# Kernel optimization log

Hardware: AMD Instinct MI355X
Metric: run time of the kernel (lower is better)

## Reference

```python
import jax, jax.numpy as jnp
import numpy as np

MASK_THR = 0.005   # cfg.mask_thr
SIGMA = 2.0        # cfg.sigma (gaussian kernel)
N, G, H, W = 500, 128, 200, 304


def setup_inputs() -> dict:
    key = jax.random.key(0)
    k1, k2, k3, k4, k5, k6 = jax.random.split(key, 6)
    return {
        "cate_scores": jax.random.uniform(k1, (N,), jnp.float32),
        "seg_preds_x": jax.random.uniform(k2, (G, H, W), jnp.float32),
        "seg_preds_y": jax.random.uniform(k3, (G, H, W), jnp.float32),
        "cate_labels": jax.random.randint(k4, (N,), 0, 80),
        "x_inds": jax.random.randint(k5, (N,), 0, G),
        "y_inds": jax.random.randint(k6, (N,), 0, G),
    }


def reference(cate_scores, seg_preds_x, seg_preds_y, cate_labels, x_inds, y_inds):
    # --- SOLO decoupled mask decoding: irregular grid-index gather ---
    mask_x = seg_preds_x[x_inds]                 # [N,H,W]
    mask_y = seg_preds_y[y_inds]                 # [N,H,W]
    soft = mask_x * mask_y                       # seg_masks_soft
    hard = (soft > MASK_THR).astype(soft.dtype)  # seg_masks (binary)
    sum_masks = hard.sum((1, 2))                 # [N] mask areas
    # mask-quality rescoring
    seg_score = (soft * hard).sum((1, 2)) / jnp.maximum(sum_masks, 1.0)
    scores = cate_scores * seg_score

    # --- Matrix NMS (gaussian kernel) ---
    flat = hard.reshape(N, -1)                   # [N, H*W]
    inter = flat @ flat.T                        # [N,N] intersection areas
    union = sum_masks[:, None] + sum_masks[None, :] - inter
    iou = jnp.triu(inter / jnp.maximum(union, 1e-6), k=1)
    label_eq = jnp.triu((cate_labels[:, None] == cate_labels[None, :]).astype(soft.dtype), k=1)
    decay_iou = iou * label_eq                   # same-class IoU, upper tri
    comp_iou = decay_iou.max(0)                  # [N] max IoU with higher-scored same-class mask
    decay_matrix = jnp.exp(-SIGMA * decay_iou ** 2)
    comp_matrix = jnp.exp(-SIGMA * comp_iou ** 2)[:, None]  # expand(n,n).T in torch
    decay_coef = (decay_matrix / comp_matrix).min(0)         # [N]
    return scores * decay_coef
```

## Files before the change

kernel.cpp:

```cpp
#include <hip/hip_runtime.h>


#define N_DET 500
#define HW    (200 * 304)
#define TILE  64
#define NT    (HW / TILE)
#define NWORDS NT
#define NW2   (NWORDS / 2)
#define LSTR  65
#define MASK_THR 0.005f
#define SIGMA 2.0f

__global__ __launch_bounds__(512) void maskgen_kernel(
    const float* __restrict__ seg_x, const float* __restrict__ seg_y,
    const int* __restrict__ x_inds, const int* __restrict__ y_inds,
    unsigned long long* __restrict__ packed,
    float* __restrict__ part_sum,
    int*   __restrict__ part_cnt)
{
    __shared__ float sx[128 * LSTR];
    __shared__ float sy[128 * LSTR];
    const int t   = blockIdx.x;
    const int tid = threadIdx.x;
    const int base_g = t * TILE;

    for (int e = tid; e < 128 * 16; e += 512) {
        const int r  = e >> 4;
        const int c4 = (e & 15) << 2;
        const float4 vx = *(const float4*)(seg_x + (size_t)r * HW + base_g + c4);
        const float4 vy = *(const float4*)(seg_y + (size_t)r * HW + base_g + c4);
        float* dx = sx + r * LSTR + c4;
        float* dy = sy + r * LSTR + c4;
        dx[0] = vx.x; dx[1] = vx.y; dx[2] = vx.z; dx[3] = vx.w;
        dy[0] = vy.x; dy[1] = vy.y; dy[2] = vy.z; dy[3] = vy.w;
    }
    __syncthreads();

    const int n = tid;
    if (n < N_DET) {
        const float* __restrict__ rx = sx + x_inds[n] * LSTR;
        const float* __restrict__ ry = sy + y_inds[n] * LSTR;
        float ssum = 0.0f;
        int   cnt  = 0;
        unsigned int lo = 0u, hi = 0u;
        #pragma unroll
        for (int p = 0; p < 32; ++p) {
            const float v = rx[p] * ry[p];
            if (v > MASK_THR) { ssum += v; ++cnt; lo |= (1u << p); }
        }
        #pragma unroll
        for (int p = 0; p < 32; ++p) {
            const float v = rx[32 + p] * ry[32 + p];
            if (v > MASK_THR) { ssum += v; ++cnt; hi |= (1u << p); }
        }
        packed[(size_t)n * NWORDS + t] = ((unsigned long long)hi << 32) | lo;
        part_sum[(size_t)t * N_DET + n] = ssum;
        part_cnt[(size_t)t * N_DET + n] = cnt;
    }
}

__global__ __launch_bounds__(64) void finalize_kernel(
    const float* __restrict__ part_sum, const int* __restrict__ part_cnt,
    const float* __restrict__ cate_scores,
    float* __restrict__ sum_masks, float* __restrict__ scores)
{
    const int n    = blockIdx.x;
    const int lane = threadIdx.x;
    float S = 0.0f; int C = 0;
    for (int t = lane; t < NT; t += 64) {
        S += part_sum[(size_t)t * N_DET + n];
        C += part_cnt[(size_t)t * N_DET + n];
    }
    #pragma unroll
    for (int off = 32; off; off >>= 1) {
        S += __shfl_down(S, off);
        C += __shfl_down(C, off);
    }
    if (lane == 0) {
        const float sm = (float)C;
        sum_masks[n] = sm;
        scores[n] = cate_scores[n] * (S / fmaxf(sm, 1.0f));
    }
}

__global__ __launch_bounds__(256) void pair_iou_kernel(
    const unsigned long long* __restrict__ packed,
    const float* __restrict__ sum_masks,
    const int* __restrict__ labels,
    float* __restrict__ d2col,
    float* __restrict__ comp2)
{
    const int j   = blockIdx.x;
    const int tid = threadIdx.x;
    const int lane = tid & 63, wav = tid >> 6;

    __shared__ int   s_lab[N_DET];
    __shared__ float s_sm[N_DET];
    __shared__ int   s_list[N_DET];
    __shared__ int   s_cnt;
    __shared__ float s_max[4];

    if (tid == 0) s_cnt = 0;
    for (int i = tid; i < N_DET; i += 256) {
        s_lab[i] = labels[i];
        s_sm[i]  = sum_masks[i];
        d2col[(size_t)j * N_DET + i] = 0.0f;
    }
    __syncthreads();

    const int   lj = s_lab[j];
    const float sj = s_sm[j];
    for (int i = tid; i < j; i += 256)
        if (s_lab[i] == lj) { const int p = atomicAdd(&s_cnt, 1); s_list[p] = i; }
    __syncthreads();
    const int cnt = s_cnt;

    const ulonglong2* __restrict__ pj2 = (const ulonglong2*)(packed + (size_t)j * NWORDS);
    ulonglong2 bj[8];
    #pragma unroll
    for (int t = 0; t < 8; ++t) {
        const int w = lane + (t << 6);
        if (w < NW2) bj[t] = pj2[w];
        else { bj[t].x = 0ull; bj[t].y = 0ull; }
    }

    float wmax = 0.0f;
    for (int p = wav; p < cnt; p += 4) {
        const int i = s_list[p];
        const ulonglong2* __restrict__ pi2 = (const ulonglong2*)(packed + (size_t)i * NWORDS);
        int part = 0;
        #pragma unroll
        for (int t = 0; t < 8; ++t) {
            const int w = lane + (t << 6);
            if (w < NW2) {
                const ulonglong2 a = pi2[w];
                part += __popcll(a.x & bj[t].x) + __popcll(a.y & bj[t].y);
            }
        }
        #pragma unroll
        for (int off = 32; off; off >>= 1) part += __shfl_down(part, off);
        if (lane == 0) {
            const float uni = s_sm[i] + sj - (float)part;
            const float iou = (float)part / fmaxf(uni, 1e-6f);
            d2col[(size_t)j * N_DET + i] = iou * iou;
            wmax = fmaxf(wmax, iou);
        }
    }
    if (lane == 0) s_max[wav] = wmax;
    __syncthreads();
    if (tid == 0) {
        const float c = fmaxf(fmaxf(s_max[0], s_max[1]), fmaxf(s_max[2], s_max[3]));
        comp2[j] = c * c;
    }
}

__global__ __launch_bounds__(64) void decay_kernel(
    const float* __restrict__ d2col,
    const float* __restrict__ comp2,
    const float* __restrict__ scores,
    float* __restrict__ out)
{
    const int j = blockIdx.x;
    const int lane = threadIdx.x;
    float m = 1e30f;
    for (int i = lane; i < N_DET; i += 64)
        m = fminf(m, comp2[i] - d2col[(size_t)j * N_DET + i]);
    #pragma unroll
    for (int off = 32; off; off >>= 1)
        m = fminf(m, __shfl_down(m, off));
    if (lane == 0) out[j] = scores[j] * expf(SIGMA * m);
}

extern "C" void kernel_launch(void* const* d_in, const int* in_sizes, int n_in,
                              void* d_out, int out_size, void* d_ws, size_t ws_size,
                              hipStream_t stream) {
    const float* cate_scores = (const float*)d_in[0];
    const float* seg_x       = (const float*)d_in[1];
    const float* seg_y       = (const float*)d_in[2];
    const int*   labels      = (const int*)d_in[3];
    const int*   x_inds      = (const int*)d_in[4];
    const int*   y_inds      = (const int*)d_in[5];
    float* out = (float*)d_out;

    char* ws = (char*)d_ws;
    unsigned long long* packed = (unsigned long long*)(ws + 0);
    float* d2col     = (float*)(ws + 3800000);
    float* part_sum  = (float*)(ws + 4800000);
    int*   part_cnt  = (int*)  (ws + 6700000);
    float* scores    = (float*)(ws + 8600000);
    float* comp2     = (float*)(ws + 8602048);
    float* sum_masks = (float*)(ws + 8604096);

    maskgen_kernel <<<NT, 512, 0, stream>>>(seg_x, seg_y, x_inds, y_inds,
                                            packed, part_sum, part_cnt);
    finalize_kernel<<<N_DET, 64, 0, stream>>>(part_sum, part_cnt, cate_scores,
                                              sum_masks, scores);
    pair_iou_kernel<<<N_DET, 256, 0, stream>>>(packed, sum_masks, labels, d2col, comp2);
    decay_kernel   <<<N_DET, 64, 0, stream>>>(d2col, comp2, scores, out);
}
```

Measured before the change: 135.1 us.

## Transpose packed mask bitsets to tile-major layout and derive counts via popcount

Packed mask bitsets move from detection-major to tile-major order with a padded stride of 512, so the mask generation kernel writes one coalesced row per tile instead of scattered per-detection writes. The separate count buffer is dropped: mask areas are now recomputed in the finalize kernel by popcounting the packed words. The finalize kernel is also regrouped so each block reduces 64 detections across 8 waves. The trade-off is that the pair-IoU kernel now reads single 64-bit words at a large stride per lane rather than contiguous 128-bit vectors, which may make its memory access less coalesced.

Result: slower. 173.5 us (+28.5%).

```diff
diff --git a/kernel.cpp b/kernel.cpp
--- a/kernel.cpp
+++ b/kernel.cpp
@@ -5,8 +5,7 @@
 #define HW    (200 * 304)
 #define TILE  64
 #define NT    (HW / TILE)
-#define NWORDS NT
-#define NW2   (NWORDS / 2)
+#define PSTR  512
 #define LSTR  65
 #define MASK_THR 0.005f
 #define SIGMA 2.0f
@@ -14,21 +13,20 @@
 __global__ __launch_bounds__(512) void maskgen_kernel(
     const float* __restrict__ seg_x, const float* __restrict__ seg_y,
     const int* __restrict__ x_inds, const int* __restrict__ y_inds,
-    unsigned long long* __restrict__ packed,
-    float* __restrict__ part_sum,
-    int*   __restrict__ part_cnt)
+    unsigned long long* __restrict__ packed_t,
+    float* __restrict__ part_sum)
 {
     __shared__ float sx[128 * LSTR];
     __shared__ float sy[128 * LSTR];
     const int t   = blockIdx.x;
     const int tid = threadIdx.x;
-    const int base_g = t * TILE;
+    const int base = t * TILE;
 
     for (int e = tid; e < 128 * 16; e += 512) {
         const int r  = e >> 4;
         const int c4 = (e & 15) << 2;
-        const float4 vx = *(const float4*)(seg_x + (size_t)r * HW + base_g + c4);
-        const float4 vy = *(const float4*)(seg_y + (size_t)r * HW + base_g + c4);
+        const float4 vx = *(const float4*)(seg_x + (size_t)r * HW + base + c4);
+        const float4 vy = *(const float4*)(seg_y + (size_t)r * HW + base + c4);
         float* dx = sx + r * LSTR + c4;
         float* dy = sy + r * LSTR + c4;
         dx[0] = vx.x; dx[1] = vx.y; dx[2] = vx.z; dx[3] = vx.w;
@@ -36,47 +34,50 @@
     }
     __syncthreads();
 
-    const int n = tid;
-    if (n < N_DET) {
-        const float* __restrict__ rx = sx + x_inds[n] * LSTR;
-        const float* __restrict__ ry = sy + y_inds[n] * LSTR;
+    if (tid < N_DET) {
+        const float* __restrict__ rx = sx + x_inds[tid] * LSTR;
+        const float* __restrict__ ry = sy + y_inds[tid] * LSTR;
         float ssum = 0.0f;
-        int   cnt  = 0;
         unsigned int lo = 0u, hi = 0u;
         #pragma unroll
         for (int p = 0; p < 32; ++p) {
             const float v = rx[p] * ry[p];
-            if (v > MASK_THR) { ssum += v; ++cnt; lo |= (1u << p); }
+            if (v > MASK_THR) { ssum += v; lo |= (1u << p); }
         }
         #pragma unroll
         for (int p = 0; p < 32; ++p) {
             const float v = rx[32 + p] * ry[32 + p];
-            if (v > MASK_THR) { ssum += v; ++cnt; hi |= (1u << p); }
+            if (v > MASK_THR) { ssum += v; hi |= (1u << p); }
         }
-        packed[(size_t)n * NWORDS + t] = ((unsigned long long)hi << 32) | lo;
-        part_sum[(size_t)t * N_DET + n] = ssum;
-        part_cnt[(size_t)t * N_DET + n] = cnt;
+        packed_t[(size_t)t * PSTR + tid] = ((unsigned long long)hi << 32) | lo;
+        part_sum[(size_t)t * PSTR + tid] = ssum;
     }
 }
 
-__global__ __launch_bounds__(64) void finalize_kernel(
-    const float* __restrict__ part_sum, const int* __restrict__ part_cnt,
+__global__ __launch_bounds__(512) void finalize_kernel(
+    const unsigned long long* __restrict__ packed_t,
+    const float* __restrict__ part_sum,
     const float* __restrict__ cate_scores,
     float* __restrict__ sum_masks, float* __restrict__ scores)
 {
-    const int n    = blockIdx.x;
-    const int lane = threadIdx.x;
+    __shared__ float sS[8][64];
+    __shared__ int   sC[8][64];
+    const int tid  = threadIdx.x;
+    const int lane = tid & 63, wav = tid >> 6;
+    const int n    = blockIdx.x * 64 + lane;
     float S = 0.0f; int C = 0;
-    for (int t = lane; t < NT; t += 64) {
-        S += part_sum[(size_t)t * N_DET + n];
-        C += part_cnt[(size_t)t * N_DET + n];
+    if (n < N_DET) {
+        for (int t = wav; t < NT; t += 8) {
+            S += part_sum[(size_t)t * PSTR + n];
+            C += __popcll(packed_t[(size_t)t * PSTR + n]);
+        }
     }
-    #pragma unroll
-    for (int off = 32; off; off >>= 1) {
-        S += __shfl_down(S, off);
-        C += __shfl_down(C, off);
-    }
-    if (lane == 0) {
+    sS[wav][lane] = S; sC[wav][lane] = C;
+    __syncthreads();
+    if (wav == 0 && n < N_DET) {
+        S = 0.0f; C = 0;
+        #pragma unroll
+        for (int q = 0; q < 8; ++q) { S += sS[q][lane]; C += sC[q][lane]; }
         const float sm = (float)C;
         sum_masks[n] = sm;
         scores[n] = cate_scores[n] * (S / fmaxf(sm, 1.0f));
@@ -84,7 +85,7 @@
 }
 
 __global__ __launch_bounds__(256) void pair_iou_kernel(
-    const unsigned long long* __restrict__ packed,
+    const unsigned long long* __restrict__ packed_t,
     const float* __restrict__ sum_masks,
     const int* __restrict__ labels,
     float* __restrict__ d2col,
@@ -115,27 +116,22 @@
     __syncthreads();
     const int cnt = s_cnt;
 
-    const ulonglong2* __restrict__ pj2 = (const ulonglong2*)(packed + (size_t)j * NWORDS);
-    ulonglong2 bj[8];
+    unsigned long long bj[15];
     #pragma unroll
-    for (int t = 0; t < 8; ++t) {
-        const int w = lane + (t << 6);
-        if (w < NW2) bj[t] = pj2[w];
-        else { bj[t].x = 0ull; bj[t].y = 0ull; }
+    for (int q = 0; q < 15; ++q) {
+        const int w = lane + (q << 6);
+        bj[q] = (w < NT) ? packed_t[(size_t)w * PSTR + j] : 0ull;
     }
 
     float wmax = 0.0f;
     for (int p = wav; p < cnt; p += 4) {
         const int i = s_list[p];
-        const ulonglong2* __restrict__ pi2 = (const ulonglong2*)(packed + (size_t)i * NWORDS);
         int part = 0;
         #pragma unroll
-        for (int t = 0; t < 8; ++t) {
-            const int w = lane + (t << 6);
-            if (w < NW2) {
-                const ulonglong2 a = pi2[w];
-                part += __popcll(a.x & bj[t].x) + __popcll(a.y & bj[t].y);
-            }
+        for (int q = 0; q < 15; ++q) {
+            const int w = lane + (q << 6);
+            if (w < NT)
+                part += __popcll(packed_t[(size_t)w * PSTR + i] & bj[q]);
         }
         #pragma unroll
         for (int off = 32; off; off >>= 1) part += __shfl_down(part, off);
@@ -183,18 +179,18 @@
     float* out = (float*)d_out;
 
     char* ws = (char*)d_ws;
-    unsigned long long* packed = (unsigned long long*)(ws + 0);
-    float* d2col     = (float*)(ws + 3800000);
-    float* part_sum  = (float*)(ws + 4800000);
-    int*   part_cnt  = (int*)  (ws + 6700000);
-    float* scores    = (float*)(ws + 8600000);
-    float* comp2     = (float*)(ws + 8602048);
-    float* sum_masks = (float*)(ws + 8604096);
+    unsigned long long* packed_t = (unsigned long long*)(ws + 0);
+    float* part_sum  = (float*)(ws + 3891200);
+    float* d2col     = (float*)(ws + 5836800);
+    float* scores    = (float*)(ws + 6836800);
+    float* comp2     = (float*)(ws + 6838800);
+    float* sum_masks = (float*)(ws + 6840800);
 
     maskgen_kernel <<<NT, 512, 0, stream>>>(seg_x, seg_y, x_inds, y_inds,
-                                            packed, part_sum, part_cnt);
-    finalize_kernel<<<N_DET, 64, 0, stream>>>(part_sum, part_cnt, cate_scores,
-                                              sum_masks, scores);
-    pair_iou_kernel<<<N_DET, 256, 0, stream>>>(packed, sum_masks, labels, d2col, comp2);
+                                            packed_t, part_sum);
+    finalize_kernel<<<8, 512, 0, stream>>>(packed_t, part_sum, cate_scores,
+                                           sum_masks, scores);
+    pair_iou_kernel<<<N_DET, 256, 0, stream>>>(packed_t, sum_masks, labels,
+                                               d2col, comp2);
     decay_kernel   <<<N_DET, 64, 0, stream>>>(d2col, comp2, scores, out);
 }
```
